# Optimization experiments

Hardware: AMD Instinct MI355X
Metric: run time of the kernel (lower is better)

## Reference

```python
import jax, jax.numpy as jnp
import numpy as np

N, D = 131072, 128
NUM_BOOK, K = 4, 1024


def setup_inputs() -> dict:
    key = jax.random.key(0)
    k1, k2 = jax.random.split(key)
    x = jax.random.normal(k1, (N, D), dtype=jnp.float32)
    codebooks = jax.random.normal(k2, (NUM_BOOK, K, D), dtype=jnp.float32)
    return {"x": x, "codebooks": codebooks}


def reference(x, codebooks):
    # Original: for each book i, idx = argmin_k cdist(x, C_i, p=2); stack -> [N, num_book].
    # argmin over Euclidean distance == argmin over squared distance, so we use
    # affect argmin). All num_book lookups batched in one einsum.
    dots = jnp.einsum('nd,bkd->bnk', x, codebooks)          # [B, N, K]
    c_sq = jnp.sum(codebooks * codebooks, axis=-1)          # [B, K]
    sq_dist = c_sq[:, None, :] - 2.0 * dots                 # [B, N, K]
    idx = jnp.argmin(sq_dist, axis=-1)                      # [B, N]
    return jnp.transpose(idx, (1, 0))                       # [N, num_book], int
```

## Files before the change

### kernel.cpp

```cpp
#include <hip/hip_runtime.h>
#include <math.h>

#define N_PTS  131072
#define DIM    128
#define NBOOK  4
#define KCODES 1024

#define CHUNK   32
#define NCHB    32
#define PT      2
#define BPTS    256
#define SLOTS   9
#define CHUNK_BYTES (SLOTS * 1024)
#define CHUNK_U16   (SLOTS * 512)
#define EPS_ACC 0.05f
#define WLB_CAP 32768

typedef _Float16 f16x8 __attribute__((ext_vector_type(8)));
typedef float    f32x16 __attribute__((ext_vector_type(16)));
typedef unsigned short u16;

#define WS_CSQ_OFF  2359296u
#define WS_CNT_OFF  (WS_CSQ_OFF + 16384u)
#define WS_WL_OFF   (WS_CNT_OFF + 256u)

__device__ inline u16 f16bits(_Float16 h) {
    union { _Float16 f; u16 u; } c; c.f = h; return c.u;
}

__device__ inline void async_copy16(const void* g, void* l) {
    __builtin_amdgcn_global_load_lds(
        (const __attribute__((address_space(1))) void*)g,
        (__attribute__((address_space(3))) void*)l,
        16, 0, 0);
}

__global__ __launch_bounds__(256)
void prep_kernel(const float* __restrict__ cb, char* __restrict__ cbf,
                 float* __restrict__ csq, int* __restrict__ counters) {
    if (blockIdx.x >= 256) {
        int idx = (blockIdx.x - 256) * 256 + threadIdx.x;
        if (idx < 4) counters[idx] = 0;
        const float4* p = (const float4*)(cb + (size_t)idx * DIM);
        float s = 0.f;
#pragma unroll
        for (int i = 0; i < DIM / 4; ++i) {
            float4 v = p[i];
            s += v.x * v.x + v.y * v.y + v.z * v.z + v.w * v.w;
        }
        csq[idx] = s;
        int b = idx >> 10, k = idx & 1023;
        _Float16 hi  = (_Float16)s;
        float    r1  = s - (float)hi;
        _Float16 mid = (_Float16)r1;
        _Float16 rem = (_Float16)(r1 - (float)mid);
        u16* dst = (u16*)(cbf + (size_t)(b * 32 + (k >> 5)) * CHUNK_BYTES
                              + 8192 + (size_t)(k & 31) * 16);
        u16 o[8] = {f16bits(hi), f16bits(mid), f16bits(rem), (u16)0x5D00, 0, 0, 0, 0};
#pragma unroll
        for (int j = 0; j < 8; ++j) dst[j] = o[j];
        u16* dz = dst + 32 * 8;
#pragma unroll
        for (int j = 0; j < 8; ++j) dz[j] = 0;
        return;
    }
    int t    = blockIdx.x * 256 + threadIdx.x;
    int lane = t & 63;
    int s    = (t >> 6) & 7;
    int bc   = t >> 9;
    int code = (bc & 31) * CHUNK + (lane & 31);
    int b    = bc >> 5;
    int dd   = s * 16 + (lane >> 5) * 8;

    const float* row = cb + ((size_t)b * KCODES + code) * DIM + dd;
    float4 v0 = ((const float4*)row)[0];
    float4 v1 = ((const float4*)row)[1];
    float vals[8] = {v0.x, v0.y, v0.z, v0.w, v1.x, v1.y, v1.z, v1.w};
    u16 o[8];
#pragma unroll
    for (int j = 0; j < 8; ++j) o[j] = f16bits((_Float16)vals[j]);
    u16* dst = (u16*)(cbf + (size_t)bc * CHUNK_BYTES + (size_t)s * 1024 + (size_t)lane * 16);
#pragma unroll
    for (int j = 0; j < 8; ++j) dst[j] = o[j];
}

__global__ __launch_bounds__(256, 3)
void argmin_mfma_kernel(const float* __restrict__ x,
                        const u16*  __restrict__ cbf,
                        int* __restrict__ out,
                        int* __restrict__ counters,
                        int* __restrict__ worklist) {
    __shared__ u16 lds[2 * CHUNK_U16];

    const int tid  = threadIdx.x;
    const int lane = tid & 63;
    const int w    = tid >> 6;
    const int n0   = blockIdx.x * BPTS;
    const int col  = lane & 31;
    const int kh   = lane >> 5;

    const char* src0 = (const char*)cbf + (size_t)(blockIdx.y * 64) * CHUNK_BYTES;

    auto issue = [&](int c) {
        const char* src = src0 + (size_t)c * CHUNK_BYTES;
        char* dst = (char*)&lds[(c & 1) * CHUNK_U16];
#pragma unroll
        for (int i = 0; i < 2; ++i)
            async_copy16(src + i * 4096 + tid * 16, dst + i * 4096 + w * 1024);
        if (w == 0)
            async_copy16(src + 8192 + lane * 16, dst + 8192);
    };

    issue(0);

    f16x8 xh[PT][8];
#pragma unroll
    for (int pt = 0; pt < PT; ++pt) {
        const float* xrow = x + (size_t)(n0 + w * 64 + pt * 32 + col) * DIM;
#pragma unroll
        for (int s = 0; s < 8; ++s) {
            const float* p = xrow + s * 16 + kh * 8;
            float4 v0 = *(const float4*)p;
            float4 v1 = *(const float4*)(p + 4);
            float vals[8] = {v0.x, v0.y, v0.z, v0.w, v1.x, v1.y, v1.z, v1.w};
            f16x8 hv;
#pragma unroll
            for (int j = 0; j < 8; ++j) hv[j] = (_Float16)vals[j];
            xh[pt][s] = hv;
        }
    }
    f16x8 xcf;
#pragma unroll
    for (int j = 0; j < 8; ++j) {
        _Float16 v = (_Float16)0.0f;
        if (kh == 0) {
            if (j < 3) v = (_Float16)(-0.5f);
            else if (j == 3) v = (_Float16)1.0f;
        }
        xcf[j] = v;
    }

    unsigned b1p[PT], b2p[PT];
    int bchunk[PT];
#pragma unroll
    for (int pt = 0; pt < PT; ++pt) { b1p[pt] = 0u; b2p[pt] = 0u; bchunk[pt] = 0; }

    auto mfma_chunk = [&](const u16* A, f32x16* ac) {
#pragma unroll
        for (int pt = 0; pt < PT; ++pt)
#pragma unroll
            for (int r = 0; r < 16; ++r) ac[pt][r] = 0.f;
#pragma unroll
        for (int s = 0; s < 8; ++s) {
            f16x8 ah = *(const f16x8*)&A[s * 512 + lane * 8];
#pragma unroll
            for (int pt = 0; pt < PT; ++pt)
                ac[pt] = __builtin_amdgcn_mfma_f32_32x32x16_f16(ah, xh[pt][s], ac[pt], 0, 0, 0);
        }
        f16x8 acs = *(const f16x8*)&A[8 * 512 + lane * 8];
#pragma unroll
        for (int pt = 0; pt < PT; ++pt)
            ac[pt] = __builtin_amdgcn_mfma_f32_32x32x16_f16(acs, xcf, ac[pt], 0, 0, 0);
    };

    auto epilogue = [&](const f32x16* ac, int cc) {
        int ci = cc & 31;
#pragma unroll
        for (int pt = 0; pt < PT; ++pt) {
            unsigned prev = b1p[pt], p1v = prev, p2v = b2p[pt];
#pragma unroll
            for (int r = 0; r < 16; r += 2) {
                unsigned pa = (__float_as_uint(ac[pt][r])     & 0xFFFFFFE0u) | (31u - (unsigned)r);
                unsigned pb = (__float_as_uint(ac[pt][r + 1]) & 0xFFFFFFE0u) | (30u - (unsigned)r);
                unsigned hi = pa > pb ? pa : pb;
                unsigned lo = pa < pb ? pa : pb;
                unsigned t2 = hi < p1v ? hi : p1v;
                unsigned m  = lo > t2 ? lo : t2;
                p2v = p2v > m ? p2v : m;
                p1v = p1v > hi ? p1v : hi;
            }
            bchunk[pt] = (p1v != prev) ? ci : bchunk[pt];
            b1p[pt] = p1v; b2p[pt] = p2v;
        }
    };

    auto finalize = [&](int book) {
        int b = blockIdx.y * 2 + book;
#pragma unroll
        for (int pt = 0; pt < PT; ++pt) {
            unsigned r = 31u - (b1p[pt] & 31u);
            float m1 = __uint_as_float(b1p[pt] & 0xFFFFFFE0u);
            float m2 = __uint_as_float(b2p[pt] & 0xFFFFFFE0u);
            int row = (int)((r & 3u) + 8u * (r >> 2)) + 4 * kh;
            int code = bchunk[pt] * CHUNK + row;
            float om1 = __shfl_xor(m1, 32);
            float om2 = __shfl_xor(m2, 32);
            int   oc  = __shfl_xor(code, 32);
            bool take = (om1 > m1) || (om1 == m1 && oc < code);
            float nm2 = fmaxf(fminf(m1, om1), fmaxf(m2, om2));
            if (take) { m1 = om1; code = oc; }
            m2 = nm2;
            if (lane < 32) {
                int point = n0 + w * 64 + pt * 32 + col;
                out[point * NBOOK + b] = code;
                if (m1 - m2 < EPS_ACC) {
                    int pos = atomicAdd(&counters[b], 1);
                    if (pos < WLB_CAP) worklist[b * WLB_CAP + pos] = point;
                }
            }
            b1p[pt] = 0u; b2p[pt] = 0u; bchunk[pt] = 0;
        }
    };

    __syncthreads();

    f32x16 acc0[PT], acc1[PT];
    for (int c = 0; c < 64; c += 2) {
        issue(c + 1);
        mfma_chunk(lds, acc0);
        if (c > 0) {
            epilogue(acc1, c - 1);
            if (c == 32) finalize(0);
        }
        __syncthreads();

        if (c + 2 < 64) issue(c + 2);
        mfma_chunk(lds + CHUNK_U16, acc1);
        epilogue(acc0, c);
        __syncthreads();
    }
    epilogue(acc1, 63);
    finalize(1);
}

__global__ __launch_bounds__(256)
void exact_kernel(const float* __restrict__ x,
                  const float* __restrict__ cb,
                  const float* __restrict__ csq,
                  const int* __restrict__ counters,
                  const int* __restrict__ worklist,
                  int* __restrict__ out) {
    const int b = blockIdx.y;
    int n = counters[b];
    if (n > WLB_CAP) n = WLB_CAP;
    const int lane = threadIdx.x & 63;
    const int w    = threadIdx.x >> 6;
    const int g    = lane >> 4;
    const int d0   = (lane & 15) * 8;
    const float* cbb = cb + (size_t)b * KCODES * DIM;
    const float* csb = csq + b * KCODES;

    for (int i = blockIdx.x * 4 + w; i < n; i += gridDim.x * 4) {
        int point = worklist[b * WLB_CAP + i];
        const float* xr = x + (size_t)point * DIM + d0;
        float4 xa = ((const float4*)xr)[0];
        float4 xb = ((const float4*)xr)[1];
        float bd = 3.4e38f;
        int   bi = 0;
#pragma unroll 4
        for (int it = 0; it < 256; ++it) {
            int c0 = it * 4 + g;
            const float* cr = cbb + (size_t)c0 * DIM + d0;
            float4 ca = ((const float4*)cr)[0];
            float4 cc = ((const float4*)cr)[1];
            float p = xa.x * ca.x + xa.y * ca.y + xa.z * ca.z + xa.w * ca.w
                    + xb.x * cc.x + xb.y * cc.y + xb.z * cc.z + xb.w * cc.w;
            p += __shfl_xor(p, 1);
            p += __shfl_xor(p, 2);
            p += __shfl_xor(p, 4);
            p += __shfl_xor(p, 8);
            float dist = csb[c0] - 2.f * p;
            if (dist < bd) { bd = dist; bi = c0; }
        }
#pragma unroll
        for (int off = 16; off <= 32; off <<= 1) {
            float od = __shfl_xor(bd, off);
            int   oi = __shfl_xor(bi, off);
            if (od < bd || (od == bd && oi < bi)) { bd = od; bi = oi; }
        }
        if (lane == 0) out[point * NBOOK + b] = bi;
    }
}

extern "C" void kernel_launch(void* const* d_in, const int* in_sizes, int n_in,
                              void* d_out, int out_size, void* d_ws, size_t ws_size,
                              hipStream_t stream) {
    const float* x  = (const float*)d_in[0];
    const float* cb = (const float*)d_in[1];
    int* out = (int*)d_out;

    char* ws = (char*)d_ws;
    u16*   cbf      = (u16*)ws;
    float* csq      = (float*)(ws + WS_CSQ_OFF);
    int*   counters = (int*)(ws + WS_CNT_OFF);
    int*   worklist = (int*)(ws + WS_WL_OFF);

    prep_kernel<<<272, 256, 0, stream>>>(cb, (char*)cbf, csq, counters);

    argmin_mfma_kernel<<<dim3(N_PTS / BPTS, 2), 256, 0, stream>>>(x, cbf, out, counters, worklist);

    exact_kernel<<<dim3(512, 4), 256, 0, stream>>>(x, cb, csq, counters, worklist, out);
}
```

Measured before the change: 371.1 us.

## Process eight worklist points per wave in exact rescoring kernel with LDS-staged x

The fp32 exact-rescore kernel now handles 8 points per wave instead of one. The x rows are staged in LDS, and each lane computes full 128-dim dot products for its own (point, code) pair, so the shuffle reduction per code is gone and each codebook load is reused across points. In exchange each lane reads a whole codebook row, giving uncoalesced, strided global loads. Padded worklist entries duplicate the last point, which causes redundant writes of identical results.

```diff
diff --git a/kernel.cpp b/kernel.cpp
--- a/kernel.cpp
+++ b/kernel.cpp
@@ -240,45 +240,61 @@
                   const int* __restrict__ counters,
                   const int* __restrict__ worklist,
                   int* __restrict__ out) {
+    __shared__ float xs[4][8][132];
+    __shared__ int   pi[4][8];
+
     const int b = blockIdx.y;
     int n = counters[b];
     if (n > WLB_CAP) n = WLB_CAP;
-    const int lane = threadIdx.x & 63;
-    const int w    = threadIdx.x >> 6;
-    const int g    = lane >> 4;
-    const int d0   = (lane & 15) * 8;
+    const int t    = threadIdx.x;
+    const int lane = t & 63;
+    const int w    = t >> 6;
+    const int ii   = lane & 7;
+    const int ci   = lane >> 3;
     const float* cbb = cb + (size_t)b * KCODES * DIM;
     const float* csb = csq + b * KCODES;
 
-    for (int i = blockIdx.x * 4 + w; i < n; i += gridDim.x * 4) {
-        int point = worklist[b * WLB_CAP + i];
-        const float* xr = x + (size_t)point * DIM + d0;
-        float4 xa = ((const float4*)xr)[0];
-        float4 xb = ((const float4*)xr)[1];
+    for (int i0 = (blockIdx.x * 4 + w) * 8; i0 < n; i0 += gridDim.x * 4 * 8) {
+        if (lane < 8) {
+            int iw = i0 + lane; if (iw >= n) iw = n - 1;
+            pi[w][lane] = worklist[b * WLB_CAP + iw];
+        }
+#pragma unroll
+        for (int p = 0; p < 4; ++p) {
+            int r  = p * 2 + (lane >> 5);
+            int ir = i0 + r; if (ir >= n) ir = n - 1;
+            int pt = worklist[b * WLB_CAP + ir];
+            float4 v = *(const float4*)(x + (size_t)pt * DIM + (lane & 31) * 4);
+            *(float4*)&xs[w][r][(lane & 31) * 4] = v;
+        }
+
+        const float* xrow = &xs[w][ii][0];
         float bd = 3.4e38f;
         int   bi = 0;
-#pragma unroll 4
-        for (int it = 0; it < 256; ++it) {
-            int c0 = it * 4 + g;
-            const float* cr = cbb + (size_t)c0 * DIM + d0;
-            float4 ca = ((const float4*)cr)[0];
-            float4 cc = ((const float4*)cr)[1];
-            float p = xa.x * ca.x + xa.y * ca.y + xa.z * ca.z + xa.w * ca.w
-                    + xb.x * cc.x + xb.y * cc.y + xb.z * cc.z + xb.w * cc.w;
-            p += __shfl_xor(p, 1);
-            p += __shfl_xor(p, 2);
-            p += __shfl_xor(p, 4);
-            p += __shfl_xor(p, 8);
-            float dist = csb[c0] - 2.f * p;
-            if (dist < bd) { bd = dist; bi = c0; }
-        }
-#pragma unroll
-        for (int off = 16; off <= 32; off <<= 1) {
+        for (int blk = 0; blk < 128; ++blk) {
+            int c = blk * 8 + ci;
+            const float* cr = cbb + (size_t)c * DIM;
+            float ax = 0.f, ay = 0.f, az = 0.f, aw = 0.f;
+#pragma unroll 8
+            for (int d = 0; d < DIM; d += 4) {
+                float4 cv = *(const float4*)(cr + d);
+                float4 xv = *(const float4*)(xrow + d);
+                ax = fmaf(cv.x, xv.x, ax);
+                ay = fmaf(cv.y, xv.y, ay);
+                az = fmaf(cv.z, xv.z, az);
+                aw = fmaf(cv.w, xv.w, aw);
+            }
+            float p = (ax + ay) + (az + aw);
+            float dist = csb[c] - 2.f * p;
+            if (dist < bd) { bd = dist; bi = c; }
+        }
+#pragma unroll
+        for (int off = 8; off <= 32; off <<= 1) {
             float od = __shfl_xor(bd, off);
             int   oi = __shfl_xor(bi, off);
             if (od < bd || (od == bd && oi < bi)) { bd = od; bi = oi; }
         }
-        if (lane == 0) out[point * NBOOK + b] = bi;
+        if (lane < 8) out[pi[w][lane] * NBOOK + b] = bi;
     }
 }
 
```

Result: slower. 688.1 us (+85.4%).

## Split exact refinement per point into eight codebook slices merged via 64-bit atomicMin

Applied to the files above, without the earlier changes.

Each ambiguous point's exact fp32 rescoring is now divided into 8 work units covering 128 codes each, instead of one wave scanning all 1024 codes. The partial minima are packed into an order-preserving 64-bit key (distance bits, then code index) and merged with atomicMin into a results buffer, which a new write kernel copies to the output. This is meant to expose more parallelism when the worklist is short and to shorten the serial tail. In exchange it adds atomics, a results buffer that must be initialised, and an extra kernel launch.

```diff
diff --git a/kernel.cpp b/kernel.cpp
--- a/kernel.cpp
+++ b/kernel.cpp
@@ -19,7 +19,9 @@
 typedef _Float16 f16x8 __attribute__((ext_vector_type(8)));
 typedef float    f32x16 __attribute__((ext_vector_type(16)));
 typedef unsigned short u16;
-
+typedef unsigned long long u64;
+
+#define WS_RES_OFF  1179648u
 #define WS_CSQ_OFF  2359296u
 #define WS_CNT_OFF  (WS_CSQ_OFF + 16384u)
 #define WS_WL_OFF   (WS_CNT_OFF + 256u)
@@ -89,7 +91,8 @@
                         const u16*  __restrict__ cbf,
                         int* __restrict__ out,
                         int* __restrict__ counters,
-                        int* __restrict__ worklist) {
+                        int* __restrict__ worklist,
+                        u64* __restrict__ results) {
     __shared__ u16 lds[2 * CHUNK_U16];
 
     const int tid  = threadIdx.x;
@@ -205,7 +208,10 @@
                 out[point * NBOOK + b] = code;
                 if (m1 - m2 < EPS_ACC) {
                     int pos = atomicAdd(&counters[b], 1);
-                    if (pos < WLB_CAP) worklist[b * WLB_CAP + pos] = point;
+                    if (pos < WLB_CAP) {
+                        worklist[b * WLB_CAP + pos] = point;
+                        results[b * WLB_CAP + pos] = 0xFFFFFFFFFFFFFFFFull;
+                    }
                 }
             }
             b1p[pt] = 0u; b2p[pt] = 0u; bchunk[pt] = 0;
@@ -239,7 +245,7 @@
                   const float* __restrict__ csq,
                   const int* __restrict__ counters,
                   const int* __restrict__ worklist,
-                  int* __restrict__ out) {
+                  u64* __restrict__ results) {
     const int b = blockIdx.y;
     int n = counters[b];
     if (n > WLB_CAP) n = WLB_CAP;
@@ -250,17 +256,20 @@
     const float* cbb = cb + (size_t)b * KCODES * DIM;
     const float* csb = csq + b * KCODES;
 
-    for (int i = blockIdx.x * 4 + w; i < n; i += gridDim.x * 4) {
+    int units = n * 8;
+    for (int u = blockIdx.x * 4 + w; u < units; u += gridDim.x * 4) {
+        int i = u >> 3, q = u & 7;
         int point = worklist[b * WLB_CAP + i];
         const float* xr = x + (size_t)point * DIM + d0;
         float4 xa = ((const float4*)xr)[0];
         float4 xb = ((const float4*)xr)[1];
         float bd = 3.4e38f;
         int   bi = 0;
+        int   c00 = q * 128;
 #pragma unroll 4
-        for (int it = 0; it < 256; ++it) {
-            int c0 = it * 4 + g;
-            const float* cr = cbb + (size_t)c0 * DIM + d0;
+        for (int it = 0; it < 32; ++it) {
+            int c = c00 + it * 4 + g;
+            const float* cr = cbb + (size_t)c * DIM + d0;
             float4 ca = ((const float4*)cr)[0];
             float4 cc = ((const float4*)cr)[1];
             float p = xa.x * ca.x + xa.y * ca.y + xa.z * ca.z + xa.w * ca.w
@@ -269,8 +278,8 @@
             p += __shfl_xor(p, 2);
             p += __shfl_xor(p, 4);
             p += __shfl_xor(p, 8);
-            float dist = csb[c0] - 2.f * p;
-            if (dist < bd) { bd = dist; bi = c0; }
+            float dist = csb[c] - 2.f * p;
+            if (dist < bd) { bd = dist; bi = c; }
         }
 #pragma unroll
         for (int off = 16; off <= 32; off <<= 1) {
@@ -278,7 +287,26 @@
             int   oi = __shfl_xor(bi, off);
             if (od < bd || (od == bd && oi < bi)) { bd = od; bi = oi; }
         }
-        if (lane == 0) out[point * NBOOK + b] = bi;
+        if (lane == 0) {
+            unsigned ub = __float_as_uint(bd);
+            ub = (ub & 0x80000000u) ? ~ub : (ub | 0x80000000u);
+            u64 key = ((u64)ub << 32) | (unsigned)bi;
+            atomicMin(&results[b * WLB_CAP + i], key);
+        }
+    }
+}
+
+__global__ __launch_bounds__(256)
+void write_kernel(const int* __restrict__ counters,
+                  const int* __restrict__ worklist,
+                  const u64* __restrict__ results,
+                  int* __restrict__ out) {
+    const int b = blockIdx.y;
+    int n = counters[b];
+    if (n > WLB_CAP) n = WLB_CAP;
+    for (int i = blockIdx.x * 256 + threadIdx.x; i < n; i += gridDim.x * 256) {
+        int point = worklist[b * WLB_CAP + i];
+        out[point * NBOOK + b] = (int)(results[b * WLB_CAP + i] & 1023u);
     }
 }
 
@@ -291,13 +319,17 @@
 
     char* ws = (char*)d_ws;
     u16*   cbf      = (u16*)ws;
+    u64*   results  = (u64*)(ws + WS_RES_OFF);
     float* csq      = (float*)(ws + WS_CSQ_OFF);
     int*   counters = (int*)(ws + WS_CNT_OFF);
     int*   worklist = (int*)(ws + WS_WL_OFF);
 
     prep_kernel<<<272, 256, 0, stream>>>(cb, (char*)cbf, csq, counters);
 
-    argmin_mfma_kernel<<<dim3(N_PTS / BPTS, 2), 256, 0, stream>>>(x, cbf, out, counters, worklist);
-
-    exact_kernel<<<dim3(512, 4), 256, 0, stream>>>(x, cb, csq, counters, worklist, out);
-}
+    argmin_mfma_kernel<<<dim3(N_PTS / BPTS, 2), 256, 0, stream>>>(x, cbf, out, counters,
+                                                                  worklist, results);
+
+    exact_kernel<<<dim3(512, 4), 256, 0, stream>>>(x, cb, csq, counters, worklist, results);
+
+    write_kernel<<<dim3(32, 4), 256, 0, stream>>>(counters, worklist, results, out);
+}
```

Result: slower. 380.4 us (+2.5%).
